# Kernel tuning notes

Hardware: AMD Instinct MI355X
Metric: run time of the kernel (lower is better)

The kernel has to match this reference:

```python
import jax, jax.numpy as jnp
import numpy as np

CHAMFER_W, NORMAL_W, EDGE_W, WATERTIGHT_W, SDF_W = 1.0, 0.5, 0.3, 0.2, 1.0
DIHEDRAL_THRESHOLD = 0.5
EPS_COS = 1e-8   # F.cosine_similarity eps
EPS_NRM = 1e-12  # F.normalize eps


def _pairwise_sqdist(p, g):
    # (B,N,3),(B,M,3) -> (B,N,M) squared distances, without (B,N,M,3) temp
    p2 = (p * p).sum(-1)
    g2 = (g * g).sum(-1)
    return p2[:, :, None] + g2[:, None, :] - 2.0 * jnp.einsum('bnd,bmd->bnm', p, g)


def _face_normals(verts, faces):
    v0, v1, v2 = verts[faces[:, 0]], verts[faces[:, 1]], verts[faces[:, 2]]
    n = jnp.cross(v1 - v0, v2 - v0)
    return n / jnp.maximum(jnp.linalg.norm(n, axis=-1, keepdims=True), EPS_NRM)


def _edge_structure(faces, num_verts):
    # All 3F directed edges (f_i, f_{(i+1)%3}), canonicalized to sorted keys.
    a = faces                      # (F,3)
    b = jnp.roll(faces, -1, axis=1)  # pairs (0,1),(1,2),(2,0)
    lo = jnp.minimum(a, b).reshape(-1)
    hi = jnp.maximum(a, b).reshape(-1)
    keys = lo * num_verts + hi      # unique int key per undirected edge (< 2^31)
    face_ids = jnp.repeat(jnp.arange(faces.shape[0], dtype=jnp.int32), 3)
    order = jnp.argsort(keys, stable=True)
    sk = keys[order]
    sf = face_ids[order]
    E = sk.shape[0]
    run_start = jnp.concatenate([jnp.array([True]), sk[1:] != sk[:-1]])
    eq_next = jnp.concatenate([sk[:-1] == sk[1:], jnp.array([False])])
    rs_pad = jnp.concatenate([run_start, jnp.array([True, True])])
    # pair2[i]: run of length exactly 2 starting at i -> faces sf[i], sf[i+1]
    pair2 = run_start & eq_next & rs_pad[2:]
    return sf, pair2, run_start


def _edge_sharpness(verts, faces):
    normals = _face_normals(verts, faces)
    sf, pair2, _ = _edge_structure(faces, verts.shape[0])
    sf_next = jnp.roll(sf, -1)
    cos = (normals[sf] * normals[sf_next]).sum(-1)
    terms = jax.nn.relu(cos - DIHEDRAL_THRESHOLD)
    cnt = pair2.sum()
    return jnp.where(cnt > 0, (terms * pair2).sum() / jnp.maximum(cnt, 1), 0.0)


def _watertight(faces, num_verts):
    _, pair2, run_start = _edge_structure(faces, num_verts)
    total = run_start.sum()
    bad = total - pair2.sum()
    return jnp.where(total > 0, bad.astype(jnp.float32) / jnp.maximum(total, 1).astype(jnp.float32), 0.0)


def setup_inputs():
    key = jax.random.key(0)
    ks = jax.random.split(key, 10)
    B, N, M, V, F, NS = 1, 8192, 8192, 20000, 40000, 65536
    return {
        'pred_sdf': jax.random.normal(ks[0], (B, NS, 1), jnp.float32),
        'gt_sdf': jax.random.normal(ks[1], (B, NS, 1), jnp.float32),
        'extracted_vertices': jax.random.normal(ks[2], (V, 3), jnp.float32),
        'extracted_faces': jax.random.randint(ks[3], (F, 3), 0, V, jnp.int32),
        'gt_vertices': jax.random.normal(ks[4], (V, 3), jnp.float32),
        'gt_faces': jax.random.randint(ks[5], (F, 3), 0, V, jnp.int32),
        'pred_points': jax.random.normal(ks[6], (B, N, 3), jnp.float32),
        'gt_points': jax.random.normal(ks[7], (B, M, 3), jnp.float32),
        'pred_normals': jax.random.normal(ks[8], (B, N, 3), jnp.float32),
        'gt_normals': jax.random.normal(ks[9], (B, M, 3), jnp.float32),
    }


def reference(pred_sdf, gt_sdf, extracted_vertices, extracted_faces, gt_vertices, gt_faces,
              pred_points, gt_points, pred_normals, gt_normals):
    # sdf supervision (L1)
    sdf_l = SDF_W * jnp.abs(pred_sdf - gt_sdf).mean()

    # chamfer
    dist = _pairwise_sqdist(pred_points, gt_points)  # (B,N,M)
    min_p2g = dist.min(axis=2).mean(axis=1)
    min_g2p = dist.min(axis=1).mean(axis=1)
    chamfer_l = CHAMFER_W * (min_p2g + min_g2p).mean()

    # normal consistency (nearest GT point per pred point)
    nn_idx = jnp.argmin(dist, axis=2)  # (B,N)
    matched = jnp.take_along_axis(gt_normals, nn_idx[..., None], axis=1)  # (B,N,3)
    pn = jnp.maximum(jnp.linalg.norm(pred_normals, axis=-1), EPS_COS)
    gn = jnp.maximum(jnp.linalg.norm(matched, axis=-1), EPS_COS)
    cos = (pred_normals * matched).sum(-1) / (pn * gn)
    normal_l = NORMAL_W * (1.0 - jnp.abs(cos)).mean()

    # edge sharpness (GT mesh args are unused by the original implementation)
    edge_l = EDGE_W * _edge_sharpness(extracted_vertices, extracted_faces)

    # watertight regularization
    wt_l = WATERTIGHT_W * _watertight(extracted_faces, extracted_vertices.shape[0])

    total = sdf_l + chamfer_l + normal_l + edge_l + wt_l
    return sdf_l, chamfer_l, normal_l, edge_l, wt_l, total
```

## Files before the change

### kernel.cpp

```cpp
#include <hip/hip_runtime.h>
#include <math.h>

#define TILE 128
#define REG 8
#define APB (256 * REG)
#define HASH_C 262144
#define HASH_MASK (HASH_C - 1)
#define EMPTY_SLOT 0xFFFFFFFFu
#define KEY_MASK ((1u << 29) - 1)
#define CNT_ONE (1u << 29)

#define SBIAS 256.0f
#define TOPBITS 0x42000000u
#define PADW 480.0f


__device__ inline float waveReduceF(float v) {
#pragma unroll
  for (int off = 32; off > 0; off >>= 1) v += __shfl_down(v, off, 64);
  return v;
}

__global__ __launch_bounds__(256) void fused_kernel(
    const float* __restrict__ P, const float* __restrict__ G, int N, int M,
    int p2gBlocks, int chamferBlocks, int nTileG, int nTileP,
    unsigned long long* __restrict__ p2g, unsigned* __restrict__ g2p,
    const float* __restrict__ verts, const int* __restrict__ faces, int F, int V,
    float4* __restrict__ fn, unsigned* __restrict__ slots,
    unsigned* __restrict__ face0, unsigned* __restrict__ face1,
    float* accumF, unsigned* accumU) {
  __shared__ float4 tile[TILE];
  int tid = threadIdx.x;

  if (blockIdx.x == 0 && tid == 0) {
#pragma unroll
    for (int q = 0; q < 7; q++) accumF[q] = 0.f;
    accumU[0] = 0u;
  }

  if ((int)blockIdx.x >= chamferBlocks) {
    int e = (blockIdx.x - chamferBlocks) * 256 + tid;
    if (e >= 3 * F) return;
    int f = e / 3, k = e - 3 * f;
    int a = faces[3 * f + k];
    int b = faces[3 * f + ((k + 1) % 3)];
    if (k == 0) {
      int i1 = faces[3 * f + 1], i2 = faces[3 * f + 2];
      float ax = verts[3 * a], ay = verts[3 * a + 1], az = verts[3 * a + 2];
      float bx = verts[3 * i1] - ax, by = verts[3 * i1 + 1] - ay, bz = verts[3 * i1 + 2] - az;
      float cx = verts[3 * i2] - ax, cy = verts[3 * i2 + 1] - ay, cz = verts[3 * i2 + 2] - az;
      float nx = by * cz - bz * cy;
      float ny = bz * cx - bx * cz;
      float nz = bx * cy - by * cx;
      float l = sqrtf(nx * nx + ny * ny + nz * nz);
      float inv = 1.f / fmaxf(l, 1e-12f);
      fn[f] = make_float4(nx * inv, ny * inv, nz * inv, 0.f);
    }
    unsigned lo = (unsigned)min(a, b), hi = (unsigned)max(a, b);
    unsigned key = lo * (unsigned)V + hi + 1u;
    unsigned h = (key * 2654435761u) & HASH_MASK;
    unsigned c;
    for (;;) {
      unsigned prev = atomicCAS(&slots[h], EMPTY_SLOT, key | CNT_ONE);
      if (prev == EMPTY_SLOT) { c = 0u; break; }
      if ((prev & KEY_MASK) == key) {
        c = (atomicAdd(&slots[h], CNT_ONE) >> 29) & 7u;
        break;
      }
      h = (h + 1) & HASH_MASK;
    }
    if (c == 0u) face0[h] = (unsigned)f;
    else if (c == 1u) face1[h] = (unsigned)f;
    return;
  }

  bool isP2G = ((int)blockIdx.x < p2gBlocks);
  const float* A;
  const float* B;
  int nA, nB, chunk, tileIdx;
  if (isP2G) {
    chunk = blockIdx.x / nTileG;
    tileIdx = blockIdx.x % nTileG;
    A = P; nA = N; B = G; nB = M;
  } else {
    int bid = blockIdx.x - p2gBlocks;
    chunk = bid / nTileP;
    tileIdx = bid % nTileP;
    A = G; nA = M; B = P; nB = N;
  }

  int abase = chunk * APB + tid;
  float px[REG], py[REG], pz[REG];
#pragma unroll
  for (int r = 0; r < REG; r++) {
    int i = abase + 256 * r;
    if (i < nA) { px[r] = A[3 * i]; py[r] = A[3 * i + 1]; pz[r] = A[3 * i + 2]; }
    else        { px[r] = 0.f; py[r] = 0.f; pz[r] = 0.f; }
  }

  int tbase = tileIdx * TILE;
  if (tid < TILE) {
    int j = tbase + tid;
    float4 v;
    if (j < nB) {
      float x = B[3 * j], y = B[3 * j + 1], z = B[3 * j + 2];
      v = make_float4(x, y, z, fmaf(0.5f, x * x + y * y + z * z, SBIAS));
    } else {
      v = make_float4(0.f, 0.f, 0.f, PADW);
    }
    tile[tid] = v;
  }
  __syncthreads();

  if (isP2G) {
    unsigned best[REG];
#pragma unroll
    for (int r = 0; r < REG; r++) best[r] = 0xFFFFFFFFu;
#pragma unroll 2
    for (int j = 0; j < TILE; j += 2) {
      float4 g0 = tile[j];
      float4 g1 = tile[j + 1];
#pragma unroll
      for (int r = 0; r < REG; r++) {
        float s0 = fmaf(-pz[r], g0.z, fmaf(-py[r], g0.y, fmaf(-px[r], g0.x, g0.w)));
        float s1 = fmaf(-pz[r], g1.z, fmaf(-py[r], g1.y, fmaf(-px[r], g1.x, g1.w)));
        unsigned k0 = (__float_as_uint(s0) << 7) | (unsigned)j;
        unsigned k1 = (__float_as_uint(s1) << 7) | (unsigned)(j + 1);
        best[r] = min(best[r], min(k0, k1));
      }
    }
#pragma unroll
    for (int r = 0; r < REG; r++) {
      int i = abase + 256 * r;
      if (i < nA) {
        unsigned sbits = (best[r] >> 7) | TOPBITS;
        unsigned idx = (unsigned)tbase + (best[r] & 127u);
        unsigned long long packed = ((unsigned long long)sbits << 32) | idx;
        atomicMin(&p2g[i], packed);
      }
    }
  } else {
    float best[REG];
#pragma unroll
    for (int r = 0; r < REG; r++) best[r] = INFINITY;
#pragma unroll 2
    for (int j = 0; j < TILE; j += 2) {
      float4 g0 = tile[j];
      float4 g1 = tile[j + 1];
#pragma unroll
      for (int r = 0; r < REG; r++) {
        float s0 = fmaf(-pz[r], g0.z, fmaf(-py[r], g0.y, fmaf(-px[r], g0.x, g0.w)));
        float s1 = fmaf(-pz[r], g1.z, fmaf(-py[r], g1.y, fmaf(-px[r], g1.x, g1.w)));
        best[r] = fminf(best[r], fminf(s0, s1));
      }
    }
#pragma unroll
    for (int r = 0; r < REG; r++) {
      int i = abase + 256 * r;
      if (i < nA) atomicMin(&g2p[i], __float_as_uint(best[r]));
    }
  }
}

__global__ __launch_bounds__(256) void finalize_kernel(
    const float* __restrict__ P, const float* __restrict__ G,
    const float* __restrict__ PN, const float* __restrict__ GN,
    const float* __restrict__ sdfA, const float* __restrict__ sdfB,
    const unsigned* __restrict__ slots, const unsigned* __restrict__ face0,
    const unsigned* __restrict__ face1, const float4* __restrict__ fn,
    int N, int M, int NS, int nBlocks,
    const unsigned long long* __restrict__ p2g, const unsigned* __restrict__ g2p,
    float* accumF, unsigned* accumU, float* out) {
  __shared__ float sh[28];
  int t = blockIdx.x * 256 + threadIdx.x;
  int stride = nBlocks * 256;
  float sp = 0.f, sg = 0.f, sn = 0.f, ss = 0.f, term = 0.f;
  unsigned runs = 0, pairs = 0;
  if (t < N) {
    unsigned long long pk = p2g[t];
    float sprime = __uint_as_float((unsigned)(pk >> 32));
    int idx = (int)(pk & 0xFFFFFFFFull);
    float px = P[3 * t], py = P[3 * t + 1], pz = P[3 * t + 2];
    sp = px * px + py * py + pz * pz + 2.f * sprime - 2.f * SBIAS;
    float nx = PN[3 * t], ny = PN[3 * t + 1], nz = PN[3 * t + 2];
    float mx = GN[3 * idx], my = GN[3 * idx + 1], mz = GN[3 * idx + 2];
    float pn = fmaxf(sqrtf(nx * nx + ny * ny + nz * nz), 1e-8f);
    float gn = fmaxf(sqrtf(mx * mx + my * my + mz * mz), 1e-8f);
    float cosv = (nx * mx + ny * my + nz * mz) / (pn * gn);
    sn = 1.f - fabsf(cosv);
  }
  if (t < M) {
    float sprime = __uint_as_float(g2p[t]);
    float gx = G[3 * t], gy = G[3 * t + 1], gz = G[3 * t + 2];
    sg = gx * gx + gy * gy + gz * gz + 2.f * sprime - 2.f * SBIAS;
  }
  for (int i = t; i < NS; i += stride) ss += fabsf(sdfA[i] - sdfB[i]);
  for (int h = t; h < HASH_C; h += stride) {
    unsigned s = slots[h];
    if (s != EMPTY_SLOT) {
      runs++;
      if ((s >> 29) == 2u) {
        pairs++;
        float4 n0 = fn[face0[h]];
        float4 n1 = fn[face1[h]];
        float c = n0.x * n1.x + n0.y * n1.y + n0.z * n1.z;
        term += fmaxf(c - 0.5f, 0.f);
      }
    }
  }
  sp = waveReduceF(sp);
  sg = waveReduceF(sg);
  sn = waveReduceF(sn);
  ss = waveReduceF(ss);
  term = waveReduceF(term);
  float fruns = waveReduceF((float)runs);
  float fpairs = waveReduceF((float)pairs);
  int lane = threadIdx.x & 63, wid = threadIdx.x >> 6;
  if (lane == 0) {
    sh[wid] = sp; sh[4 + wid] = sg; sh[8 + wid] = sn; sh[12 + wid] = ss;
    sh[16 + wid] = term; sh[20 + wid] = fruns; sh[24 + wid] = fpairs;
  }
  __syncthreads();
  if (threadIdx.x == 0) {
    atomicAdd(&accumF[1], sh[0] + sh[1] + sh[2] + sh[3]);
    atomicAdd(&accumF[2], sh[4] + sh[5] + sh[6] + sh[7]);
    atomicAdd(&accumF[3], sh[8] + sh[9] + sh[10] + sh[11]);
    atomicAdd(&accumF[0], sh[12] + sh[13] + sh[14] + sh[15]);
    atomicAdd(&accumF[4], sh[16] + sh[17] + sh[18] + sh[19]);
    atomicAdd(&accumF[5], sh[20] + sh[21] + sh[22] + sh[23]);
    atomicAdd(&accumF[6], sh[24] + sh[25] + sh[26] + sh[27]);
    __threadfence();
    unsigned ticket = atomicAdd(&accumU[0], 1u);
    if (ticket == (unsigned)(nBlocks - 1)) {
      float a0 = atomicAdd(&accumF[0], 0.f);
      float a1 = atomicAdd(&accumF[1], 0.f);
      float a2 = atomicAdd(&accumF[2], 0.f);
      float a3 = atomicAdd(&accumF[3], 0.f);
      float a4 = atomicAdd(&accumF[4], 0.f);
      float runsF = atomicAdd(&accumF[5], 0.f);
      float pairsF = atomicAdd(&accumF[6], 0.f);
      float sdf = a0 / (float)NS;
      float chamfer = a1 / (float)N + a2 / (float)M;
      float normal = 0.5f * (a3 / (float)N);
      float edge = (pairsF > 0.f) ? 0.3f * (a4 / pairsF) : 0.f;
      float wt = (runsF > 0.f) ? 0.2f * ((runsF - pairsF) / runsF) : 0.f;
      out[0] = sdf;
      out[1] = chamfer;
      out[2] = normal;
      out[3] = edge;
      out[4] = wt;
      out[5] = sdf + chamfer + normal + edge + wt;
    }
  }
}

extern "C" void kernel_launch(void* const* d_in, const int* in_sizes, int n_in,
                              void* d_out, int out_size, void* d_ws,
                              size_t ws_size, hipStream_t stream) {
  const float* pred_sdf = (const float*)d_in[0];
  const float* gt_sdf   = (const float*)d_in[1];
  const float* ev       = (const float*)d_in[2];
  const int*   ef       = (const int*)d_in[3];
  const float* pp       = (const float*)d_in[6];
  const float* gp       = (const float*)d_in[7];
  const float* pn       = (const float*)d_in[8];
  const float* gn       = (const float*)d_in[9];
  int NS = in_sizes[0];
  int V = in_sizes[2] / 3;
  int F = in_sizes[3] / 3;
  int N = in_sizes[6] / 3;
  int M = in_sizes[7] / 3;
  float* out = (float*)d_out;

  char* ws = (char*)d_ws;
  size_t offSlots = 0;
  size_t offP2G = offSlots + (size_t)HASH_C * 4;
  size_t offG2P = offP2G + (size_t)N * 8;
  size_t ffBytes = offG2P + (size_t)M * 4;
  size_t offAccumF = (ffBytes + 63) & ~(size_t)63;
  size_t offAccumU = offAccumF + 32;
  size_t offFace0 = offAccumU + 32;
  size_t offFace1 = offFace0 + (size_t)HASH_C * 4;
  size_t offFN = (offFace1 + (size_t)HASH_C * 4 + 15) & ~(size_t)15;

  unsigned* slots = (unsigned*)(ws + offSlots);
  unsigned long long* p2gArr = (unsigned long long*)(ws + offP2G);
  unsigned* g2pArr = (unsigned*)(ws + offG2P);
  float* accumF = (float*)(ws + offAccumF);
  unsigned* accumU = (unsigned*)(ws + offAccumU);
  unsigned* face0 = (unsigned*)(ws + offFace0);
  unsigned* face1 = (unsigned*)(ws + offFace1);
  float4* fnorm = (float4*)(ws + offFN);

  hipMemsetAsync(ws, 0xFF, ffBytes, stream);

  int nChunkP = (N + APB - 1) / APB, nTileG = (M + TILE - 1) / TILE;
  int nChunkG = (M + APB - 1) / APB, nTileP = (N + TILE - 1) / TILE;
  int p2gBlocks = nChunkP * nTileG;
  int chamferBlocks = p2gBlocks + nChunkG * nTileP;
  int meshBlocks = (3 * F + 255) / 256;
  fused_kernel<<<chamferBlocks + meshBlocks, 256, 0, stream>>>(
      pp, gp, N, M, p2gBlocks, chamferBlocks, nTileG, nTileP, p2gArr, g2pArr,
      ev, ef, F, V, fnorm, slots, face0, face1, accumF, accumU);

  int mx = (N > M ? N : M);
  int nFin = (mx + 255) / 256;
  if (nFin < 128) nFin = 128;
  finalize_kernel<<<nFin, 256, 0, stream>>>(
      pp, gp, pn, gn, pred_sdf, gt_sdf, slots, face0, face1, fnorm,
      N, M, NS, nFin, p2gArr, g2pArr, accumF, accumU, out);
}
```

Baseline: 117.5 us.

## Compact mesh edge pairs into a list and count runs with ballots

The mesh hashing pass now runs first in the grid. It records slots that become shared edges into a compact pair list and accumulates distinct-edge and pair counts through wave ballots plus atomics. Finalize then walks only that list instead of scanning the whole 262144-slot hash table, so the run/pair reductions go away. The chamfer inner loop is also unrolled to four tile points per step, and the finalize block floor drops from 128 to 64. The costs are extra global atomics on the counter words and a list that also picks up slots later upgraded to a count of three, which are filtered again at read time.

Result: slower. 120.4 us (+2.4%).

```diff
diff --git a/kernel.cpp b/kernel.cpp
--- a/kernel.cpp
+++ b/kernel.cpp
@@ -23,69 +23,86 @@
 
 __global__ __launch_bounds__(256) void fused_kernel(
     const float* __restrict__ P, const float* __restrict__ G, int N, int M,
-    int p2gBlocks, int chamferBlocks, int nTileG, int nTileP,
+    int meshBlocks, int p2gBlocks, int nTileG, int nTileP,
     unsigned long long* __restrict__ p2g, unsigned* __restrict__ g2p,
     const float* __restrict__ verts, const int* __restrict__ faces, int F, int V,
     float4* __restrict__ fn, unsigned* __restrict__ slots,
     unsigned* __restrict__ face0, unsigned* __restrict__ face1,
+    unsigned* __restrict__ cnt, unsigned* __restrict__ pairList,
     float* accumF, unsigned* accumU) {
   __shared__ float4 tile[TILE];
   int tid = threadIdx.x;
 
   if (blockIdx.x == 0 && tid == 0) {
 #pragma unroll
-    for (int q = 0; q < 7; q++) accumF[q] = 0.f;
+    for (int q = 0; q < 5; q++) accumF[q] = 0.f;
     accumU[0] = 0u;
   }
 
-  if ((int)blockIdx.x >= chamferBlocks) {
-    int e = (blockIdx.x - chamferBlocks) * 256 + tid;
-    if (e >= 3 * F) return;
-    int f = e / 3, k = e - 3 * f;
-    int a = faces[3 * f + k];
-    int b = faces[3 * f + ((k + 1) % 3)];
-    if (k == 0) {
-      int i1 = faces[3 * f + 1], i2 = faces[3 * f + 2];
-      float ax = verts[3 * a], ay = verts[3 * a + 1], az = verts[3 * a + 2];
-      float bx = verts[3 * i1] - ax, by = verts[3 * i1 + 1] - ay, bz = verts[3 * i1 + 2] - az;
-      float cx = verts[3 * i2] - ax, cy = verts[3 * i2 + 1] - ay, cz = verts[3 * i2 + 2] - az;
-      float nx = by * cz - bz * cy;
-      float ny = bz * cx - bx * cz;
-      float nz = bx * cy - by * cx;
-      float l = sqrtf(nx * nx + ny * ny + nz * nz);
-      float inv = 1.f / fmaxf(l, 1e-12f);
-      fn[f] = make_float4(nx * inv, ny * inv, nz * inv, 0.f);
-    }
-    unsigned lo = (unsigned)min(a, b), hi = (unsigned)max(a, b);
-    unsigned key = lo * (unsigned)V + hi + 1u;
-    unsigned h = (key * 2654435761u) & HASH_MASK;
-    unsigned c;
-    for (;;) {
-      unsigned prev = atomicCAS(&slots[h], EMPTY_SLOT, key | CNT_ONE);
-      if (prev == EMPTY_SLOT) { c = 0u; break; }
-      if ((prev & KEY_MASK) == key) {
-        c = (atomicAdd(&slots[h], CNT_ONE) >> 29) & 7u;
-        break;
-      }
-      h = (h + 1) & HASH_MASK;
-    }
-    if (c == 0u) face0[h] = (unsigned)f;
-    else if (c == 1u) face1[h] = (unsigned)f;
+  if ((int)blockIdx.x < meshBlocks) {
+    int e = blockIdx.x * 256 + tid;
+    bool valid = (e < 3 * F);
+    unsigned c = 0xFFu;
+    if (valid) {
+      int f = e / 3, k = e - 3 * f;
+      int a = faces[3 * f + k];
+      int b = faces[3 * f + ((k + 1) % 3)];
+      if (k == 0) {
+        int i1 = faces[3 * f + 1], i2 = faces[3 * f + 2];
+        float ax = verts[3 * a], ay = verts[3 * a + 1], az = verts[3 * a + 2];
+        float bx = verts[3 * i1] - ax, by = verts[3 * i1 + 1] - ay, bz = verts[3 * i1 + 2] - az;
+        float cx = verts[3 * i2] - ax, cy = verts[3 * i2 + 1] - ay, cz = verts[3 * i2 + 2] - az;
+        float nx = by * cz - bz * cy;
+        float ny = bz * cx - bx * cz;
+        float nz = bx * cy - by * cx;
+        float l = sqrtf(nx * nx + ny * ny + nz * nz);
+        float inv = 1.f / fmaxf(l, 1e-12f);
+        fn[f] = make_float4(nx * inv, ny * inv, nz * inv, 0.f);
+      }
+      unsigned lo = (unsigned)min(a, b), hi = (unsigned)max(a, b);
+      unsigned key = lo * (unsigned)V + hi + 1u;
+      unsigned h = (key * 2654435761u) & HASH_MASK;
+      for (;;) {
+        unsigned prev = atomicCAS(&slots[h], EMPTY_SLOT, key | CNT_ONE);
+        if (prev == EMPTY_SLOT) { c = 0u; break; }
+        if ((prev & KEY_MASK) == key) {
+          c = (atomicAdd(&slots[h], CNT_ONE) >> 29) & 7u;
+          break;
+        }
+        h = (h + 1) & HASH_MASK;
+      }
+      if (c == 0u) face0[h] = (unsigned)f;
+      else if (c == 1u) {
+        face1[h] = (unsigned)f;
+        unsigned idx = atomicAdd(&cnt[2], 1u) + 1u;
+        pairList[idx] = h;
+      }
+    }
+    unsigned long long b0 = __ballot(valid && c == 0u);
+    unsigned long long b1 = __ballot(valid && c == 1u);
+    unsigned long long b2 = __ballot(valid && c == 2u);
+    if ((tid & 63) == 0) {
+      unsigned d = (unsigned)__popcll(b0);
+      unsigned pd = (unsigned)__popcll(b1) - (unsigned)__popcll(b2);
+      if (d) atomicAdd(&cnt[0], d);
+      if (pd) atomicAdd(&cnt[1], pd);
+    }
     return;
   }
 
-  bool isP2G = ((int)blockIdx.x < p2gBlocks);
+  int bid = blockIdx.x - meshBlocks;
+  bool isP2G = (bid < p2gBlocks);
   const float* A;
   const float* B;
   int nA, nB, chunk, tileIdx;
   if (isP2G) {
-    chunk = blockIdx.x / nTileG;
-    tileIdx = blockIdx.x % nTileG;
+    chunk = bid / nTileG;
+    tileIdx = bid % nTileG;
     A = P; nA = N; B = G; nB = M;
   } else {
-    int bid = blockIdx.x - p2gBlocks;
-    chunk = bid / nTileP;
-    tileIdx = bid % nTileP;
+    int b2 = bid - p2gBlocks;
+    chunk = b2 / nTileP;
+    tileIdx = b2 % nTileP;
     A = G; nA = M; B = P; nB = N;
   }
 
@@ -117,16 +134,22 @@
 #pragma unroll
     for (int r = 0; r < REG; r++) best[r] = 0xFFFFFFFFu;
 #pragma unroll 2
-    for (int j = 0; j < TILE; j += 2) {
+    for (int j = 0; j < TILE; j += 4) {
       float4 g0 = tile[j];
       float4 g1 = tile[j + 1];
+      float4 g2 = tile[j + 2];
+      float4 g3 = tile[j + 3];
 #pragma unroll
       for (int r = 0; r < REG; r++) {
         float s0 = fmaf(-pz[r], g0.z, fmaf(-py[r], g0.y, fmaf(-px[r], g0.x, g0.w)));
         float s1 = fmaf(-pz[r], g1.z, fmaf(-py[r], g1.y, fmaf(-px[r], g1.x, g1.w)));
+        float s2 = fmaf(-pz[r], g2.z, fmaf(-py[r], g2.y, fmaf(-px[r], g2.x, g2.w)));
+        float s3 = fmaf(-pz[r], g3.z, fmaf(-py[r], g3.y, fmaf(-px[r], g3.x, g3.w)));
         unsigned k0 = (__float_as_uint(s0) << 7) | (unsigned)j;
         unsigned k1 = (__float_as_uint(s1) << 7) | (unsigned)(j + 1);
-        best[r] = min(best[r], min(k0, k1));
+        unsigned k2 = (__float_as_uint(s2) << 7) | (unsigned)(j + 2);
+        unsigned k3 = (__float_as_uint(s3) << 7) | (unsigned)(j + 3);
+        best[r] = min(min(best[r], min(k0, k1)), min(k2, k3));
       }
     }
 #pragma unroll
@@ -144,14 +167,18 @@
 #pragma unroll
     for (int r = 0; r < REG; r++) best[r] = INFINITY;
 #pragma unroll 2
-    for (int j = 0; j < TILE; j += 2) {
+    for (int j = 0; j < TILE; j += 4) {
       float4 g0 = tile[j];
       float4 g1 = tile[j + 1];
+      float4 g2 = tile[j + 2];
+      float4 g3 = tile[j + 3];
 #pragma unroll
       for (int r = 0; r < REG; r++) {
         float s0 = fmaf(-pz[r], g0.z, fmaf(-py[r], g0.y, fmaf(-px[r], g0.x, g0.w)));
         float s1 = fmaf(-pz[r], g1.z, fmaf(-py[r], g1.y, fmaf(-px[r], g1.x, g1.w)));
-        best[r] = fminf(best[r], fminf(s0, s1));
+        float s2 = fmaf(-pz[r], g2.z, fmaf(-py[r], g2.y, fmaf(-px[r], g2.x, g2.w)));
+        float s3 = fmaf(-pz[r], g3.z, fmaf(-py[r], g3.y, fmaf(-px[r], g3.x, g3.w)));
+        best[r] = fminf(fminf(best[r], fminf(s0, s1)), fminf(s2, s3));
       }
     }
 #pragma unroll
@@ -168,14 +195,14 @@
     const float* __restrict__ sdfA, const float* __restrict__ sdfB,
     const unsigned* __restrict__ slots, const unsigned* __restrict__ face0,
     const unsigned* __restrict__ face1, const float4* __restrict__ fn,
+    const unsigned* __restrict__ cnt, const unsigned* __restrict__ pairList,
     int N, int M, int NS, int nBlocks,
     const unsigned long long* __restrict__ p2g, const unsigned* __restrict__ g2p,
     float* accumF, unsigned* accumU, float* out) {
-  __shared__ float sh[28];
+  __shared__ float sh[20];
   int t = blockIdx.x * 256 + threadIdx.x;
   int stride = nBlocks * 256;
   float sp = 0.f, sg = 0.f, sn = 0.f, ss = 0.f, term = 0.f;
-  unsigned runs = 0, pairs = 0;
   if (t < N) {
     unsigned long long pk = p2g[t];
     float sprime = __uint_as_float((unsigned)(pk >> 32));
@@ -195,17 +222,14 @@
     sg = gx * gx + gy * gy + gz * gz + 2.f * sprime - 2.f * SBIAS;
   }
   for (int i = t; i < NS; i += stride) ss += fabsf(sdfA[i] - sdfB[i]);
-  for (int h = t; h < HASH_C; h += stride) {
-    unsigned s = slots[h];
-    if (s != EMPTY_SLOT) {
-      runs++;
-      if ((s >> 29) == 2u) {
-        pairs++;
-        float4 n0 = fn[face0[h]];
-        float4 n1 = fn[face1[h]];
-        float c = n0.x * n1.x + n0.y * n1.y + n0.z * n1.z;
-        term += fmaxf(c - 0.5f, 0.f);
-      }
+  unsigned listLen = cnt[2] + 1u;
+  for (unsigned i = (unsigned)t; i < listLen; i += (unsigned)stride) {
+    unsigned h = pairList[i];
+    if ((slots[h] >> 29) == 2u) {
+      float4 n0 = fn[face0[h]];
+      float4 n1 = fn[face1[h]];
+      float c = n0.x * n1.x + n0.y * n1.y + n0.z * n1.z;
+      term += fmaxf(c - 0.5f, 0.f);
     }
   }
   sp = waveReduceF(sp);
@@ -213,12 +237,10 @@
   sn = waveReduceF(sn);
   ss = waveReduceF(ss);
   term = waveReduceF(term);
-  float fruns = waveReduceF((float)runs);
-  float fpairs = waveReduceF((float)pairs);
   int lane = threadIdx.x & 63, wid = threadIdx.x >> 6;
   if (lane == 0) {
     sh[wid] = sp; sh[4 + wid] = sg; sh[8 + wid] = sn; sh[12 + wid] = ss;
-    sh[16 + wid] = term; sh[20 + wid] = fruns; sh[24 + wid] = fpairs;
+    sh[16 + wid] = term;
   }
   __syncthreads();
   if (threadIdx.x == 0) {
@@ -227,8 +249,6 @@
     atomicAdd(&accumF[3], sh[8] + sh[9] + sh[10] + sh[11]);
     atomicAdd(&accumF[0], sh[12] + sh[13] + sh[14] + sh[15]);
     atomicAdd(&accumF[4], sh[16] + sh[17] + sh[18] + sh[19]);
-    atomicAdd(&accumF[5], sh[20] + sh[21] + sh[22] + sh[23]);
-    atomicAdd(&accumF[6], sh[24] + sh[25] + sh[26] + sh[27]);
     __threadfence();
     unsigned ticket = atomicAdd(&accumU[0], 1u);
     if (ticket == (unsigned)(nBlocks - 1)) {
@@ -237,8 +257,8 @@
       float a2 = atomicAdd(&accumF[2], 0.f);
       float a3 = atomicAdd(&accumF[3], 0.f);
       float a4 = atomicAdd(&accumF[4], 0.f);
-      float runsF = atomicAdd(&accumF[5], 0.f);
-      float pairsF = atomicAdd(&accumF[6], 0.f);
+      float runsF = (float)(cnt[0] + 1u);
+      float pairsF = (float)(cnt[1] + 1u);
       float sdf = a0 / (float)NS;
       float chamfer = a1 / (float)N + a2 / (float)M;
       float normal = 0.5f * (a3 / (float)N);
@@ -276,21 +296,25 @@
   size_t offSlots = 0;
   size_t offP2G = offSlots + (size_t)HASH_C * 4;
   size_t offG2P = offP2G + (size_t)N * 8;
-  size_t ffBytes = offG2P + (size_t)M * 4;
+  size_t offCnt = offG2P + (size_t)M * 4;
+  size_t ffBytes = offCnt + 16;
   size_t offAccumF = (ffBytes + 63) & ~(size_t)63;
   size_t offAccumU = offAccumF + 32;
   size_t offFace0 = offAccumU + 32;
   size_t offFace1 = offFace0 + (size_t)HASH_C * 4;
   size_t offFN = (offFace1 + (size_t)HASH_C * 4 + 15) & ~(size_t)15;
+  size_t offPairList = offFN + (size_t)F * 16;
 
   unsigned* slots = (unsigned*)(ws + offSlots);
   unsigned long long* p2gArr = (unsigned long long*)(ws + offP2G);
   unsigned* g2pArr = (unsigned*)(ws + offG2P);
+  unsigned* cnt = (unsigned*)(ws + offCnt);
   float* accumF = (float*)(ws + offAccumF);
   unsigned* accumU = (unsigned*)(ws + offAccumU);
   unsigned* face0 = (unsigned*)(ws + offFace0);
   unsigned* face1 = (unsigned*)(ws + offFace1);
   float4* fnorm = (float4*)(ws + offFN);
+  unsigned* pairList = (unsigned*)(ws + offPairList);
 
   hipMemsetAsync(ws, 0xFF, ffBytes, stream);
 
@@ -299,14 +323,14 @@
   int p2gBlocks = nChunkP * nTileG;
   int chamferBlocks = p2gBlocks + nChunkG * nTileP;
   int meshBlocks = (3 * F + 255) / 256;
-  fused_kernel<<<chamferBlocks + meshBlocks, 256, 0, stream>>>(
-      pp, gp, N, M, p2gBlocks, chamferBlocks, nTileG, nTileP, p2gArr, g2pArr,
-      ev, ef, F, V, fnorm, slots, face0, face1, accumF, accumU);
+  fused_kernel<<<meshBlocks + chamferBlocks, 256, 0, stream>>>(
+      pp, gp, N, M, meshBlocks, p2gBlocks, nTileG, nTileP, p2gArr, g2pArr,
+      ev, ef, F, V, fnorm, slots, face0, face1, cnt, pairList, accumF, accumU);
 
   int mx = (N > M ? N : M);
   int nFin = (mx + 255) / 256;
-  if (nFin < 128) nFin = 128;
+  if (nFin < 64) nFin = 64;
   finalize_kernel<<<nFin, 256, 0, stream>>>(
       pp, gp, pn, gn, pred_sdf, gt_sdf, slots, face0, face1, fnorm,
-      N, M, NS, nFin, p2gArr, g2pArr, accumF, accumU, out);
+      cnt, pairList, N, M, NS, nFin, p2gArr, g2pArr, accumF, accumU, out);
 }
```
